# Kernel tuning notes

Measured on AMD Instinct MI355X. Metric: run time of the kernel, lower is better.

## Reference

```python
import jax, jax.numpy as jnp
from jax import lax
import numpy as np

B, T, F, H, L, HOR = 512, 512, 16, 256, 3, 24


def setup_inputs() -> dict:
    key = jax.random.key(0)
    ks = jax.random.split(key, 9)
    s = 0.05
    x = jax.random.normal(ks[0], (B, T, F), dtype=jnp.float32)
    # PyTorch LSTM params: gate order (i, f, g, o), W_ih [4H, in], W_hh [4H, H]
    W_ih0 = jax.random.normal(ks[1], (4 * H, F), dtype=jnp.float32) * s
    W_ih12 = jax.random.normal(ks[2], (L - 1, 4 * H, H), dtype=jnp.float32) * s
    W_hh = jax.random.normal(ks[3], (L, 4 * H, H), dtype=jnp.float32) * s
    b_ih = jax.random.normal(ks[4], (L, 4 * H), dtype=jnp.float32) * s
    b_hh = jax.random.normal(ks[5], (L, 4 * H), dtype=jnp.float32) * s
    fc_W = jax.random.normal(ks[6], (HOR, H), dtype=jnp.float32) * s
    fc_b = jax.random.normal(ks[7], (HOR,), dtype=jnp.float32) * s
    return {"x": x, "W_ih0": W_ih0, "W_ih12": W_ih12, "W_hh": W_hh,
            "b_ih": b_ih, "b_hh": b_hh, "fc_W": fc_W, "fc_b": fc_b}


def _lstm_layer(x, W_ih, W_hh, b_ih, b_hh):
    # x: [B, T, in] -> h sequence [B, T, H]
    Bn = x.shape[0]
    Hn = W_hh.shape[1]
    # precompute input contribution for all timesteps (one big GEMM)
    xg = jnp.einsum('bti,gi->btg', x, W_ih) + b_ih  # [B, T, 4H]
    W_hh_T = W_hh.T  # [H, 4H]

    def step(carry, xg_t):
        h, c = carry
        gates = xg_t + h @ W_hh_T + b_hh  # [B, 4H]
        i, f, g, o = jnp.split(gates, 4, axis=-1)
        c = jax.nn.sigmoid(f) * c + jax.nn.sigmoid(i) * jnp.tanh(g)
        h = jax.nn.sigmoid(o) * jnp.tanh(c)
        return (h, c), h

    h0 = jnp.zeros((Bn, Hn), x.dtype)
    c0 = jnp.zeros((Bn, Hn), x.dtype)
    _, hs = lax.scan(step, (h0, c0), jnp.swapaxes(xg, 0, 1))  # [T, B, H]
    return jnp.swapaxes(hs, 0, 1)


def reference(x, W_ih0, W_ih12, W_hh, b_ih, b_hh, fc_W, fc_b):
    h = _lstm_layer(x, W_ih0, W_hh[0], b_ih[0], b_hh[0])
    for l in range(1, L):
        h = _lstm_layer(h, W_ih12[l - 1], W_hh[l], b_ih[l], b_hh[l])
    last_hidden = h[:, -1, :]  # [B, H]
    return last_hidden @ fc_W.T + fc_b  # [B, horizon]
```

## Files before the change

### kernel.cpp

```cpp
#include <hip/hip_runtime.h>
#include <hip/hip_bf16.h>
#include <stdint.h>

#define Bsz 512
#define Tsz 512
#define Fsz 16
#define Hsz 256
#define HORZ 24

#define NG 8
#define NBT 8
#define BT 64
#define USL 32
#define PD 8
#define HBUF_ELEMS ((size_t)3*PD*Bsz*Hsz)
#define NFLAGS (3*NG*NBT)
#define AROW_B 512
#define ABUF_B (BT*AROW_B)
#define HTILE_B (BT*64)
#define SMEM_B (3*ABUF_B + HTILE_B)

#define POISON   0x7FC07FC0u
#define POISON64 0x7FC07FC07FC07FC0ull

typedef float  f32x4  __attribute__((ext_vector_type(4)));
typedef float  f32x16 __attribute__((ext_vector_type(16)));
typedef __bf16 bf16x8 __attribute__((ext_vector_type(8)));
typedef uint32_t u32x2 __attribute__((ext_vector_type(2)));
typedef uint32_t u32x4 __attribute__((ext_vector_type(4)));

__device__ __forceinline__ float sigm(float v){ return 1.f/(1.f+__expf(-v)); }

__device__ __forceinline__ bf16x8 ld_sc01_b128(const void* p){
  bf16x8 r;
  asm volatile("global_load_dwordx4 %0, %1, off sc0 sc1" : "=&v"(r) : "v"(p) : "memory");
  return r;
}
__device__ __forceinline__ u32x2 ld_b64_async(const void* p){
  u32x2 r;
  asm volatile("global_load_dwordx2 %0, %1, off" : "=&v"(r) : "v"(p) : "memory");
  return r;
}
__device__ __forceinline__ void st_sc01_b64(void* p, uint64_t v){
  asm volatile("global_store_dwordx2 %0, %1, off sc0 sc1" :: "v"(p), "v"(v) : "memory");
}
__device__ __forceinline__ void st_sc01_b32(void* p, uint32_t v){
  asm volatile("global_store_dword %0, %1, off sc0 sc1" :: "v"(p), "v"(v) : "memory");
}
__device__ __forceinline__ uint32_t ld_sc01_b32(const void* p){
  uint32_t r;
  asm volatile("global_load_dword %0, %1, off sc0 sc1\n\ts_waitcnt vmcnt(0)"
    : "=&v"(r) : "v"(p) : "memory");
  return r;
}
__device__ __forceinline__ void wait_flag(const unsigned int* fp, int target){
  int guard = 0;
  while ((int)ld_sc01_b32(fp) < target){
    __builtin_amdgcn_s_sleep(1);
    if (++guard > (1<<18)) break;
  }
}
__device__ __forceinline__ bool poison_free(const bf16x8* v){
  bool ok = true;
  #pragma unroll
  for (int j=0;j<4;++j){
    u32x4 uv = __builtin_bit_cast(u32x4, v[j]);
    ok = ok && (uv[0] != POISON) && (uv[2] != POISON);
  }
  return ok;
}
__device__ __forceinline__ void poll_load4(bf16x8* dst, const __bf16* src){
  int guard = 0;
  for(;;){
    #pragma unroll
    for (int j=0;j<4;++j) dst[j] = ld_sc01_b128(src + j*8);
    asm volatile("s_waitcnt vmcnt(0)" ::: "memory");
    __builtin_amdgcn_sched_barrier(0);
    if (poison_free(dst)) break;
    __builtin_amdgcn_s_sleep(1);
    if (++guard > (1<<16)) break;
  }
}

template<bool L0>
__device__ __forceinline__ void lstm_body(
    int l, int g, int nb, int tid,
    const float* __restrict__ xin,
    const float* __restrict__ Wih0,
    const float* __restrict__ Wih12,
    const float* __restrict__ Whh,
    const float* __restrict__ bih,
    const float* __restrict__ bhh,
    __bf16* __restrict__ hb,
    unsigned int* __restrict__ flags,
    char* smem)
{
  char* ain0  = smem;
  char* ain1  = smem + ABUF_B;
  char* hrc   = smem + 2*ABUF_B;
  char* htile = smem + 3*ABUF_B;

  const int lane = tid & 63;
  const int wid  = tid >> 6;
  const int wm   = wid >> 2;
  const int wn   = wid & 3;
  const int b0   = nb * BT;
  const int m0   = wm * 32;
  const int n0   = wn * 32;

  const int colL = n0 + (lane & 31);
  const int hi   = lane >> 5;
  const int kg8  = hi * 8;
  const int kg16 = hi * 16;
  const int R    = (colL&3)*Hsz + g*USL + (colL>>2);
  const float bias = bih[l*4*Hsz + R] + bhh[l*4*Hsz + R];
  const int rowA = m0 + (lane & 31);
  const int swzA = (rowA & 7) << 4;

  constexpr int NC = L0 ? 17 : 32;
  bf16x8 w[NC];
  {
    const float* recB = Whh + ((size_t)l*4*Hsz + R)*Hsz;
    #pragma unroll
    for (int c=0;c<NC;++c){
      const float* p;
      if constexpr (L0) p = (c==0) ? (Wih0 + (size_t)R*Fsz + kg8)
                                   : (recB + (c-1)*16 + kg8);
      else              p = (c<16) ? (Wih12 + ((size_t)(l-1)*4*Hsz + R)*Hsz + c*16 + kg8)
                                   : (recB + (c-16)*16 + kg8);
      f32x4 u0 = *(const f32x4*)p;
      f32x4 u1 = *(const f32x4*)(p+4);
      bf16x8 t;
      #pragma unroll
      for (int j=0;j<4;++j){ t[j]=(__bf16)u0[j]; t[j+4]=(__bf16)u1[j]; }
      w[c] = t;
    }
  }

  const int srow = tid >> 3, sq = tid & 7;
  const int sswz = (srow & 7) << 4;
  const size_t sgrow = (size_t)(b0 + srow) * Hsz;

  float cst[16];
  #pragma unroll
  for (int i=0;i<16;++i) cst[i]=0.f;

  unsigned int* myflag = flags + ((l*NG+g)*NBT + nb);
  const bool q2 = ((colL & 3) == 2);
  auto slotp = [&](int ll, int s){ return hb + ((size_t)ll*PD + (s&(PD-1)))*Bsz*Hsz; };

  {
    u32x4 z = {0,0,0,0};
    #pragma unroll
    for (int j=0;j<4;++j) *(u32x4*)(hrc + tid*64 + j*16) = z;
  }
  if constexpr (L0){
    u32x2 xv = ld_b64_async(xin + ((size_t)(b0+srow)*Tsz + 0)*Fsz + sq*2);
    asm volatile("s_waitcnt vmcnt(0)" ::: "memory");
    __builtin_amdgcn_sched_barrier(0);
    char* d = ain0 + srow*32 + sq*4;
    *(__bf16*)(d)   = (__bf16)__uint_as_float(xv[0]);
    *(__bf16*)(d+2) = (__bf16)__uint_as_float(xv[1]);
  } else {
    bf16x8 av[4];
    poll_load4(av, slotp(l-1,0) + sgrow + sq*32);
    #pragma unroll
    for (int j=0;j<4;++j)
      *(bf16x8*)(ain0 + srow*AROW_B + ((sq*64 + j*16) ^ sswz)) = av[j];
  }
  __syncthreads();

  for (int t=0; t<Tsz; ++t){
    char* aprd = (t&1) ? ain1 : ain0;
    char* apwr = (t&1) ? ain0 : ain1;

    if (l < 2 && (t & 3) == 0 && t >= 4 && tid < 8)
      wait_flag(flags + (((l+1)*NG + tid)*NBT + nb), t-3);

    bf16x8 hiv[4]; const __bf16* pfsrc = nullptr;
    const bool pfon = (!L0) && (t+1 < Tsz);
    if constexpr (L0){
      u32x2 xv = ld_b64_async(xin + ((size_t)(b0+srow)*Tsz + t)*Fsz + sq*2);
      bf16x8 hrv[4];
      if (t > 0) poll_load4(hrv, slotp(l,t-1) + sgrow + sq*32);
      else { asm volatile("s_waitcnt vmcnt(0)" ::: "memory");
             __builtin_amdgcn_sched_barrier(0); }
      char* d = ain0 + srow*32 + sq*4;
      *(__bf16*)(d)   = (__bf16)__uint_as_float(xv[0]);
      *(__bf16*)(d+2) = (__bf16)__uint_as_float(xv[1]);
      if (t > 0){
        #pragma unroll
        for (int j=0;j<4;++j)
          *(bf16x8*)(hrc + srow*AROW_B + ((sq*64 + j*16) ^ sswz)) = hrv[j];
      }
    } else {
      if (t > 0){
        bf16x8 hrv[4];
        poll_load4(hrv, slotp(l,t-1) + sgrow + sq*32);
        #pragma unroll
        for (int j=0;j<4;++j)
          *(bf16x8*)(hrc + srow*AROW_B + ((sq*64 + j*16) ^ sswz)) = hrv[j];
      }
      if (pfon){
        pfsrc = slotp(l-1,t+1) + sgrow + sq*32;
        #pragma unroll
        for (int j=0;j<4;++j) hiv[j] = ld_sc01_b128(pfsrc + j*8);
      }
    }
    __syncthreads();

    f32x16 acc;
    #pragma unroll
    for (int i=0;i<16;++i) acc[i]=0.f;
    #pragma unroll
    for (int c=0;c<NC;++c){
      bf16x8 af;
      if constexpr (L0){
        if (c==0) af = *(const bf16x8*)(ain0 + rowA*32 + kg16);
        else      af = *(const bf16x8*)(hrc + rowA*AROW_B + ((((c-1)*32) + kg16) ^ swzA));
      } else {
        if (c<16) af = *(const bf16x8*)(aprd + rowA*AROW_B + (((c*32) + kg16) ^ swzA));
        else      af = *(const bf16x8*)(hrc  + rowA*AROW_B + ((((c-16)*32) + kg16) ^ swzA));
      }
      acc = __builtin_amdgcn_mfma_f32_32x32x16_bf16(af, w[c], acc, 0,0,0);
    }

    #pragma unroll
    for (int i=0;i<16;++i){
      float v  = acc[i] + bias;
      float vv = q2 ? 2.f*v : v;
      float sg = sigm(vv);
      float act = q2 ? (2.f*sg - 1.f) : sg;
      float a1 = __shfl_xor(act,1,64);
      float a2 = __shfl_xor(act,2,64);
      float a3 = __shfl_xor(act,3,64);
      if ((lane&3)==0){
        float cn = a1*cst[i] + act*a2;
        cst[i] = cn;
        float th = 2.f*sigm(2.f*cn) - 1.f;
        float hv = a3*th;
        int r = (i&3) + 8*(i>>2) + 4*hi;
        int unit = colL >> 2;
        *(__bf16*)(htile + (m0 + r)*64 + unit*2) = (__bf16)hv;
      }
    }
    __syncthreads();

    if (pfon){
      asm volatile("s_waitcnt vmcnt(0)" ::: "memory");
      __builtin_amdgcn_sched_barrier(0);
      if (!poison_free(hiv)) poll_load4(hiv, pfsrc);
      #pragma unroll
      for (int j=0;j<4;++j)
        *(bf16x8*)(apwr + srow*AROW_B + ((sq*64 + j*16) ^ sswz)) = hiv[j];
    }
    __syncthreads();
    {
      uint64_t v = *(const uint64_t*)(htile + srow*64 + sq*8);
      st_sc01_b64(slotp(l,t)   + sgrow + g*USL + sq*4, v);
      st_sc01_b64(slotp(l,t+2) + sgrow + g*USL + sq*4, POISON64);
    }
    if (tid==0) st_sc01_b32(myflag, (uint32_t)(t+1));
  }
}

__global__ __launch_bounds__(512, 2) void lstm_persist(
    const float* __restrict__ xin,
    const float* __restrict__ Wih0,
    const float* __restrict__ Wih12,
    const float* __restrict__ Whh,
    const float* __restrict__ bih,
    const float* __restrict__ bhh,
    __bf16* __restrict__ hb,
    unsigned int* __restrict__ flags)
{
  __shared__ __align__(16) char smem[SMEM_B];
  const int bid = blockIdx.x;
  const int l   = bid >> 6;
  const int g   = (bid >> 3) & 7;
  const int nb  = bid & 7;
  const int tid = threadIdx.x;
  if (l == 0)
    lstm_body<true >(l,g,nb,tid, xin,Wih0,Wih12,Whh,bih,bhh, hb,flags, smem);
  else
    lstm_body<false>(l,g,nb,tid, xin,Wih0,Wih12,Whh,bih,bhh, hb,flags, smem);
}

__global__ void init_ws(uint32_t* __restrict__ hb32, uint32_t* __restrict__ flags)
{
  size_t i = (size_t)blockIdx.x*blockDim.x + threadIdx.x;
  size_t n = (HBUF_ELEMS*2)/16;
  if (i < n){
    u32x4 v = {POISON, POISON, POISON, POISON};
    *(u32x4*)(hb32 + i*4) = v;
  }
  if (i < NFLAGS) flags[i] = 0;
}

__global__ void fc_kernel(const __bf16* __restrict__ hb,
                          const float* __restrict__ fcW,
                          const float* __restrict__ fcb,
                          float* __restrict__ out)
{
  __shared__ float hs[Hsz];
  int b = blockIdx.x;
  const __bf16* hp = hb + ((size_t)(2*PD + ((Tsz-1)&(PD-1))))*Bsz*Hsz + (size_t)b*Hsz;
  for (int i = threadIdx.x; i < Hsz; i += 64) hs[i] = (float)hp[i];
  __syncthreads();
  int o = threadIdx.x;
  if (o < HORZ) {
    float a = fcb[o];
    #pragma unroll 8
    for (int u=0; u<Hsz; ++u) a += hs[u]*fcW[o*Hsz + u];
    out[b*HORZ + o] = a;
  }
}

extern "C" void kernel_launch(void* const* d_in, const int* in_sizes, int n_in,
                              void* d_out, int out_size, void* d_ws, size_t ws_size,
                              hipStream_t stream)
{
  const float* x     = (const float*)d_in[0];
  const float* Wih0  = (const float*)d_in[1];
  const float* Wih12 = (const float*)d_in[2];
  const float* Whh   = (const float*)d_in[3];
  const float* bih   = (const float*)d_in[4];
  const float* bhh   = (const float*)d_in[5];
  const float* fcW   = (const float*)d_in[6];
  const float* fcb   = (const float*)d_in[7];

  __bf16* hb = (__bf16*)d_ws;
  unsigned int* flags = (unsigned int*)((char*)d_ws + HBUF_ELEMS*2);

  size_t nchunk = (HBUF_ELEMS*2)/16;
  int ib = (int)((nchunk + 255) / 256);
  hipLaunchKernelGGL(init_ws, dim3(ib), dim3(256), 0, stream, (uint32_t*)hb, flags);

  hipLaunchKernelGGL(lstm_persist, dim3(3*NG*NBT), dim3(512), 0, stream,
                     x, Wih0, Wih12, Whh, bih, bhh, hb, flags);
  hipLaunchKernelGGL(fc_kernel, dim3(Bsz), dim3(64), 0, stream, hb, fcW, fcb, (float*)d_out);
}
```

Baseline: 3.283 ms.

## Split batch tile into two half-tiles with interleaved prefetch and 16x16 MFMAs

Each timestep now processes the 64-row batch tile as two 32-row halves, using 16x16x32 MFMAs in place of 32x32x16. While one half computes, the global loads for the other half's recurrent state and input are issued early, so polling latency overlaps with compute. The poison slot written ahead moves from t+2 to t+1, and the shared-memory layout is rebuilt with per-half buffers. The risks are more barriers per step, a changed poison and prefetch protocol that may race, and different register pressure.

```diff
diff --git a/kernel.cpp b/kernel.cpp
--- a/kernel.cpp
+++ b/kernel.cpp
@@ -11,22 +11,18 @@
 #define NG 8
 #define NBT 8
 #define BT 64
+#define HR 32
 #define USL 32
 #define PD 8
 #define HBUF_ELEMS ((size_t)3*PD*Bsz*Hsz)
 #define NFLAGS (3*NG*NBT)
-#define AROW_B 512
-#define ABUF_B (BT*AROW_B)
-#define HTILE_B (BT*64)
-#define SMEM_B (3*ABUF_B + HTILE_B)
+#define SMEM_B (84*1024)
 
 #define POISON   0x7FC07FC0u
 #define POISON64 0x7FC07FC07FC07FC0ull
 
 typedef float  f32x4  __attribute__((ext_vector_type(4)));
-typedef float  f32x16 __attribute__((ext_vector_type(16)));
 typedef __bf16 bf16x8 __attribute__((ext_vector_type(8)));
-typedef uint32_t u32x2 __attribute__((ext_vector_type(2)));
 typedef uint32_t u32x4 __attribute__((ext_vector_type(4)));
 
 __device__ __forceinline__ float sigm(float v){ return 1.f/(1.f+__expf(-v)); }
@@ -36,9 +32,9 @@
   asm volatile("global_load_dwordx4 %0, %1, off sc0 sc1" : "=&v"(r) : "v"(p) : "memory");
   return r;
 }
-__device__ __forceinline__ u32x2 ld_b64_async(const void* p){
-  u32x2 r;
-  asm volatile("global_load_dwordx2 %0, %1, off" : "=&v"(r) : "v"(p) : "memory");
+__device__ __forceinline__ uint32_t ld_b32_async(const void* p){
+  uint32_t r;
+  asm volatile("global_load_dword %0, %1, off" : "=&v"(r) : "v"(p) : "memory");
   return r;
 }
 __device__ __forceinline__ void st_sc01_b64(void* p, uint64_t v){
@@ -60,27 +56,105 @@
     if (++guard > (1<<18)) break;
   }
 }
-__device__ __forceinline__ bool poison_free(const bf16x8* v){
-  bool ok = true;
-  #pragma unroll
-  for (int j=0;j<4;++j){
-    u32x4 uv = __builtin_bit_cast(u32x4, v[j]);
-    ok = ok && (uv[0] != POISON) && (uv[2] != POISON);
-  }
-  return ok;
-}
-__device__ __forceinline__ void poll_load4(bf16x8* dst, const __bf16* src){
+__device__ __forceinline__ bool pf_ok2(const bf16x8* v){
+  u32x4 a = __builtin_bit_cast(u32x4, v[0]);
+  u32x4 b = __builtin_bit_cast(u32x4, v[1]);
+  return (a[0]!=POISON) & (a[2]!=POISON) & (b[0]!=POISON) & (b[2]!=POISON);
+}
+__device__ __forceinline__ void poll_load2(bf16x8* d, const __bf16* src){
   int guard = 0;
   for(;;){
-    #pragma unroll
-    for (int j=0;j<4;++j) dst[j] = ld_sc01_b128(src + j*8);
+    d[0] = ld_sc01_b128(src);
+    d[1] = ld_sc01_b128(src + 8);
     asm volatile("s_waitcnt vmcnt(0)" ::: "memory");
     __builtin_amdgcn_sched_barrier(0);
-    if (poison_free(dst)) break;
+    if (pf_ok2(d)) break;
     __builtin_amdgcn_s_sleep(1);
     if (++guard > (1<<16)) break;
   }
 }
+
+#define HALF_ITER(T, TY, RB, RBN, HRCX, AINX, HTX, CSTX, HRV, HIV, XV, HRVN, HIVN, XVN) \
+  {                                                                                     \
+    if ((T) > 0){                                                                       \
+      asm volatile("s_waitcnt vmcnt(0)" ::: "memory");                                  \
+      __builtin_amdgcn_sched_barrier(0);                                                \
+      if (!pf_ok2(HRV))                                                                 \
+        poll_load2(HRV, slotp(l,(T)-1) + (size_t)(b0+(RB)+sr)*Hsz + sq*16);             \
+      *(bf16x8*)((HRCX) + sr*512 + ((sq*32)    ^ skey)) = (HRV)[0];                     \
+      *(bf16x8*)((HRCX) + sr*512 + ((sq*32+16) ^ skey)) = (HRV)[1];                     \
+      if constexpr (L0){                                                                \
+        *(__bf16*)((AINX) + sr*64 + sq*2) = (__bf16)__uint_as_float(XV);                \
+      } else {                                                                          \
+        if (!pf_ok2(HIV))                                                               \
+          poll_load2(HIV, slotp(l-1,(T)) + (size_t)(b0+(RB)+sr)*Hsz + sq*16);           \
+        *(bf16x8*)((AINX) + sr*512 + ((sq*32)    ^ skey)) = (HIV)[0];                   \
+        *(bf16x8*)((AINX) + sr*512 + ((sq*32+16) ^ skey)) = (HIV)[1];                   \
+      }                                                                                 \
+    }                                                                                   \
+    __syncthreads();                                                                    \
+    f32x4 acc0, acc1;                                                                   \
+    acc0[0]=0.f;acc0[1]=0.f;acc0[2]=0.f;acc0[3]=0.f;                                    \
+    acc1[0]=0.f;acc1[1]=0.f;acc1[2]=0.f;acc1[3]=0.f;                                    \
+    _Pragma("unroll")                                                                   \
+    for (int c=0;c<NC;++c){                                                             \
+      bf16x8 a0, a1;                                                                    \
+      if constexpr (L0){                                                                \
+        if (c==0){ a0 = *(const bf16x8*)((AINX) + r0*64 + kq16);                        \
+                   a1 = *(const bf16x8*)((AINX) + r1*64 + kq16); }                      \
+        else { int off = (((c-1)*64) + kq16) ^ akey;                                    \
+               a0 = *(const bf16x8*)((HRCX) + r0*512 + off);                            \
+               a1 = *(const bf16x8*)((HRCX) + r1*512 + off); }                          \
+      } else {                                                                          \
+        const char* bse = (c<8) ? (AINX) : (HRCX);                                     \
+        int cc = (c<8) ? c : c-8;                                                       \
+        int off = ((cc*64) + kq16) ^ akey;                                              \
+        a0 = *(const bf16x8*)(bse + r0*512 + off);                                      \
+        a1 = *(const bf16x8*)(bse + r1*512 + off);                                      \
+      }                                                                                 \
+      acc0 = __builtin_amdgcn_mfma_f32_16x16x32_bf16(a0, w[c], acc0, 0,0,0);            \
+      acc1 = __builtin_amdgcn_mfma_f32_16x16x32_bf16(a1, w[c], acc1, 0,0,0);            \
+    }                                                                                   \
+    _Pragma("unroll")                                                                   \
+    for (int mt=0; mt<2; ++mt){                                                         \
+      _Pragma("unroll")                                                                 \
+      for (int rr=0; rr<4; ++rr){                                                       \
+        float v  = (mt ? acc1[rr] : acc0[rr]) + bias;                                   \
+        float vv = q2 ? 2.f*v : v;                                                      \
+        float sg = sigm(vv);                                                            \
+        float act = q2 ? (2.f*sg - 1.f) : sg;                                           \
+        float a1f = __shfl_xor(act,1,64);                                               \
+        float a2f = __shfl_xor(act,2,64);                                               \
+        float a3f = __shfl_xor(act,3,64);                                               \
+        if (gate==0){                                                                   \
+          float cn = a1f*(CSTX)[mt*4+rr] + act*a2f;                                     \
+          (CSTX)[mt*4+rr] = cn;                                                         \
+          float hv = a3f*(2.f*sigm(2.f*cn) - 1.f);                                      \
+          int rh = mt*16 + kq*4 + rr;                                                   \
+          *(__bf16*)((HTX) + rh*64 + unit*2) = (__bf16)hv;                              \
+        }                                                                               \
+      }                                                                                 \
+    }                                                                                   \
+    __syncthreads();                                                                    \
+    if (tid < 256){                                                                     \
+      int row = tid>>3, q = tid&7;                                                      \
+      uint64_t v = *(const uint64_t*)((HTX) + row*64 + q*8);                            \
+      st_sc01_b64(slotp(l,(T))   + (size_t)(b0+(RB)+row)*Hsz + g*USL + q*4, v);         \
+      st_sc01_b64(slotp(l,(T)+1) + (size_t)(b0+(RB)+row)*Hsz + g*USL + q*4, POISON64);  \
+    }                                                                                   \
+    if ((TY) >= 1 && (TY) < Tsz){                                                       \
+      const __bf16* pa = slotp(l,(TY)-1) + (size_t)(b0+(RBN)+sr)*Hsz + sq*16;           \
+      (HRVN)[0] = ld_sc01_b128(pa);                                                     \
+      (HRVN)[1] = ld_sc01_b128(pa + 8);                                                 \
+      if constexpr (L0){                                                                \
+        XVN = ld_b32_async(xin + ((size_t)(b0+(RBN)+sr)*Tsz + (TY))*Fsz + sq);          \
+      } else {                                                                          \
+        const __bf16* pb = slotp(l-1,(TY)) + (size_t)(b0+(RBN)+sr)*Hsz + sq*16;         \
+        (HIVN)[0] = ld_sc01_b128(pb);                                                   \
+        (HIVN)[1] = ld_sc01_b128(pb + 8);                                               \
+      }                                                                                 \
+    }                                                                                   \
+  }
 
 template<bool L0>
 __device__ __forceinline__ void lstm_body(
@@ -95,171 +169,104 @@
     unsigned int* __restrict__ flags,
     char* smem)
 {
-  char* ain0  = smem;
-  char* ain1  = smem + ABUF_B;
-  char* hrc   = smem + 2*ABUF_B;
-  char* htile = smem + 3*ABUF_B;
+  constexpr int ASZ = L0 ? (HR*64) : (HR*512);
+  char* hrc0 = smem;
+  char* hrc1 = smem + HR*512;
+  char* ain0 = smem + 2*HR*512;
+  char* ain1 = ain0 + ASZ;
+  char* ht0  = ain1 + ASZ;
+  char* ht1  = ht0 + HR*64;
 
   const int lane = tid & 63;
   const int wid  = tid >> 6;
-  const int wm   = wid >> 2;
-  const int wn   = wid & 3;
   const int b0   = nb * BT;
-  const int m0   = wm * 32;
-  const int n0   = wn * 32;
-
-  const int colL = n0 + (lane & 31);
-  const int hi   = lane >> 5;
-  const int kg8  = hi * 8;
-  const int kg16 = hi * 16;
-  const int R    = (colL&3)*Hsz + g*USL + (colL>>2);
+  const int colL = wid*16 + (lane & 15);
+  const int kq   = lane >> 4;
+  const int kq16 = kq * 16;
+  const int gate = colL & 3;
+  const int unit = colL >> 2;
+  const int R    = gate*Hsz + g*USL + unit;
   const float bias = bih[l*4*Hsz + R] + bhh[l*4*Hsz + R];
-  const int rowA = m0 + (lane & 31);
-  const int swzA = (rowA & 7) << 4;
-
-  constexpr int NC = L0 ? 17 : 32;
+  const bool q2 = (gate == 2);
+  const int r0 = lane & 15, r1 = 16 + (lane & 15);
+  const int akey = (lane & 7) << 4;
+
+  const int sr = tid >> 4, sq = tid & 15;
+  const int skey = (sr & 7) << 4;
+
+  constexpr int NC = L0 ? 9 : 16;
+  const int kg8 = kq * 8;
   bf16x8 w[NC];
   {
     const float* recB = Whh + ((size_t)l*4*Hsz + R)*Hsz;
     #pragma unroll
     for (int c=0;c<NC;++c){
-      const float* p;
-      if constexpr (L0) p = (c==0) ? (Wih0 + (size_t)R*Fsz + kg8)
-                                   : (recB + (c-1)*16 + kg8);
-      else              p = (c<16) ? (Wih12 + ((size_t)(l-1)*4*Hsz + R)*Hsz + c*16 + kg8)
-                                   : (recB + (c-16)*16 + kg8);
-      f32x4 u0 = *(const f32x4*)p;
-      f32x4 u1 = *(const f32x4*)(p+4);
       bf16x8 t;
-      #pragma unroll
-      for (int j=0;j<4;++j){ t[j]=(__bf16)u0[j]; t[j+4]=(__bf16)u1[j]; }
+      if constexpr (L0){
+        if (c==0){
+          if (kg8 < Fsz){
+            const float* p = Wih0 + (size_t)R*Fsz + kg8;
+            #pragma unroll
+            for (int j=0;j<8;++j) t[j] = (__bf16)p[j];
+          } else {
+            #pragma unroll
+            for (int j=0;j<8;++j) t[j] = (__bf16)0.f;
+          }
+        } else {
+          const float* p = recB + (c-1)*32 + kg8;
+          #pragma unroll
+          for (int j=0;j<8;++j) t[j] = (__bf16)p[j];
+        }
+      } else {
+        const float* p = (c<8) ? (Wih12 + ((size_t)(l-1)*4*Hsz + R)*Hsz + c*32 + kg8)
+                               : (recB + (c-8)*32 + kg8);
+        #pragma unroll
+        for (int j=0;j<8;++j) t[j] = (__bf16)p[j];
+      }
       w[c] = t;
     }
   }
 
-  const int srow = tid >> 3, sq = tid & 7;
-  const int sswz = (srow & 7) << 4;
-  const size_t sgrow = (size_t)(b0 + srow) * Hsz;
-
-  float cst[16];
+  float cst0[8], cst1[8];
   #pragma unroll
-  for (int i=0;i<16;++i) cst[i]=0.f;
+  for (int i=0;i<8;++i){ cst0[i]=0.f; cst1[i]=0.f; }
 
   unsigned int* myflag = flags + ((l*NG+g)*NBT + nb);
-  const bool q2 = ((colL & 3) == 2);
   auto slotp = [&](int ll, int s){ return hb + ((size_t)ll*PD + (s&(PD-1)))*Bsz*Hsz; };
 
   {
     u32x4 z = {0,0,0,0};
     #pragma unroll
-    for (int j=0;j<4;++j) *(u32x4*)(hrc + tid*64 + j*16) = z;
+    for (int j=0;j<4;++j) *(u32x4*)(smem + tid*64 + j*16) = z;
   }
   if constexpr (L0){
-    u32x2 xv = ld_b64_async(xin + ((size_t)(b0+srow)*Tsz + 0)*Fsz + sq*2);
-    asm volatile("s_waitcnt vmcnt(0)" ::: "memory");
-    __builtin_amdgcn_sched_barrier(0);
-    char* d = ain0 + srow*32 + sq*4;
-    *(__bf16*)(d)   = (__bf16)__uint_as_float(xv[0]);
-    *(__bf16*)(d+2) = (__bf16)__uint_as_float(xv[1]);
+    *(uint64_t*)(ain0 + tid*8) = 0;
+    __syncthreads();
+    float xa = xin[((size_t)(b0 +      sr)*Tsz + 0)*Fsz + sq];
+    float xb = xin[((size_t)(b0 + HR + sr)*Tsz + 0)*Fsz + sq];
+    *(__bf16*)(ain0 + sr*64 + sq*2) = (__bf16)xa;
+    *(__bf16*)(ain1 + sr*64 + sq*2) = (__bf16)xb;
   } else {
-    bf16x8 av[4];
-    poll_load4(av, slotp(l-1,0) + sgrow + sq*32);
-    #pragma unroll
-    for (int j=0;j<4;++j)
-      *(bf16x8*)(ain0 + srow*AROW_B + ((sq*64 + j*16) ^ sswz)) = av[j];
+    bf16x8 tmp[2];
+    poll_load2(tmp, slotp(l-1,0) + (size_t)(b0 + sr)*Hsz + sq*16);
+    *(bf16x8*)(ain0 + sr*512 + ((sq*32)    ^ skey)) = tmp[0];
+    *(bf16x8*)(ain0 + sr*512 + ((sq*32+16) ^ skey)) = tmp[1];
+    poll_load2(tmp, slotp(l-1,0) + (size_t)(b0 + HR + sr)*Hsz + sq*16);
+    *(bf16x8*)(ain1 + sr*512 + ((sq*32)    ^ skey)) = tmp[0];
+    *(bf16x8*)(ain1 + sr*512 + ((sq*32+16) ^ skey)) = tmp[1];
   }
   __syncthreads();
 
+  bf16x8 hrvA[2], hrvB[2], hivA[2], hivB[2];
+  uint32_t xvA=0, xvB=0;
+
   for (int t=0; t<Tsz; ++t){
-    char* aprd = (t&1) ? ain1 : ain0;
-    char* apwr = (t&1) ? ain0 : ain1;
-
     if (l < 2 && (t & 3) == 0 && t >= 4 && tid < 8)
       wait_flag(flags + (((l+1)*NG + tid)*NBT + nb), t-3);
 
-    bf16x8 hiv[4]; const __bf16* pfsrc = nullptr;
-    const bool pfon = (!L0) && (t+1 < Tsz);
-    if constexpr (L0){
-      u32x2 xv = ld_b64_async(xin + ((size_t)(b0+srow)*Tsz + t)*Fsz + sq*2);
-      bf16x8 hrv[4];
-      if (t > 0) poll_load4(hrv, slotp(l,t-1) + sgrow + sq*32);
-      else { asm volatile("s_waitcnt vmcnt(0)" ::: "memory");
-             __builtin_amdgcn_sched_barrier(0); }
-      char* d = ain0 + srow*32 + sq*4;
-      *(__bf16*)(d)   = (__bf16)__uint_as_float(xv[0]);
-      *(__bf16*)(d+2) = (__bf16)__uint_as_float(xv[1]);
-      if (t > 0){
-        #pragma unroll
-        for (int j=0;j<4;++j)
-          *(bf16x8*)(hrc + srow*AROW_B + ((sq*64 + j*16) ^ sswz)) = hrv[j];
-      }
-    } else {
-      if (t > 0){
-        bf16x8 hrv[4];
-        poll_load4(hrv, slotp(l,t-1) + sgrow + sq*32);
-        #pragma unroll
-        for (int j=0;j<4;++j)
-          *(bf16x8*)(hrc + srow*AROW_B + ((sq*64 + j*16) ^ sswz)) = hrv[j];
-      }
-      if (pfon){
-        pfsrc = slotp(l-1,t+1) + sgrow + sq*32;
-        #pragma unroll
-        for (int j=0;j<4;++j) hiv[j] = ld_sc01_b128(pfsrc + j*8);
-      }
-    }
-    __syncthreads();
-
-    f32x16 acc;
-    #pragma unroll
-    for (int i=0;i<16;++i) acc[i]=0.f;
-    #pragma unroll
-    for (int c=0;c<NC;++c){
-      bf16x8 af;
-      if constexpr (L0){
-        if (c==0) af = *(const bf16x8*)(ain0 + rowA*32 + kg16);
-        else      af = *(const bf16x8*)(hrc + rowA*AROW_B + ((((c-1)*32) + kg16) ^ swzA));
-      } else {
-        if (c<16) af = *(const bf16x8*)(aprd + rowA*AROW_B + (((c*32) + kg16) ^ swzA));
-        else      af = *(const bf16x8*)(hrc  + rowA*AROW_B + ((((c-16)*32) + kg16) ^ swzA));
-      }
-      acc = __builtin_amdgcn_mfma_f32_32x32x16_bf16(af, w[c], acc, 0,0,0);
-    }
-
-    #pragma unroll
-    for (int i=0;i<16;++i){
-      float v  = acc[i] + bias;
-      float vv = q2 ? 2.f*v : v;
-      float sg = sigm(vv);
-      float act = q2 ? (2.f*sg - 1.f) : sg;
-      float a1 = __shfl_xor(act,1,64);
-      float a2 = __shfl_xor(act,2,64);
-      float a3 = __shfl_xor(act,3,64);
-      if ((lane&3)==0){
-        float cn = a1*cst[i] + act*a2;
-        cst[i] = cn;
-        float th = 2.f*sigm(2.f*cn) - 1.f;
-        float hv = a3*th;
-        int r = (i&3) + 8*(i>>2) + 4*hi;
-        int unit = colL >> 2;
-        *(__bf16*)(htile + (m0 + r)*64 + unit*2) = (__bf16)hv;
-      }
-    }
-    __syncthreads();
-
-    if (pfon){
-      asm volatile("s_waitcnt vmcnt(0)" ::: "memory");
-      __builtin_amdgcn_sched_barrier(0);
-      if (!poison_free(hiv)) poll_load4(hiv, pfsrc);
-      #pragma unroll
-      for (int j=0;j<4;++j)
-        *(bf16x8*)(apwr + srow*AROW_B + ((sq*64 + j*16) ^ sswz)) = hiv[j];
-    }
-    __syncthreads();
-    {
-      uint64_t v = *(const uint64_t*)(htile + srow*64 + sq*8);
-      st_sc01_b64(slotp(l,t)   + sgrow + g*USL + sq*4, v);
-      st_sc01_b64(slotp(l,t+2) + sgrow + g*USL + sq*4, POISON64);
-    }
+    HALF_ITER(t, t,   0,  HR, hrc0, ain0, ht0, cst0, hrvA, hivA, xvA, hrvB, hivB, xvB);
+    HALF_ITER(t, t+1, HR, 0,  hrc1, ain1, ht1, cst1, hrvB, hivB, xvB, hrvA, hivA, xvA);
+
     if (tid==0) st_sc01_b32(myflag, (uint32_t)(t+1));
   }
 }
```

Result: slower. 3.508 ms (+6.9%).

## Process two batch tiles per block and overlap one tile's loads with other's compute

Applied to the files above, without the earlier changes.

Each persistent block now owns two 64-row batch tiles (X and Y) instead of one, halving the grid to 96 blocks. Within each timestep the block alternates tiles, issuing the global loads for the other tile's recurrent and input state before computing the current tile, so the exchange latency is hidden behind MFMA work. This also amortizes the register-resident weights over twice the batch. The cost is more shared memory per block (136KB), fewer blocks in flight, and a longer serial chain per timestep in each block.

```diff
diff --git a/kernel.cpp b/kernel.cpp
--- a/kernel.cpp
+++ b/kernel.cpp
@@ -9,16 +9,13 @@
 #define HORZ 24
 
 #define NG 8
-#define NBT 8
+#define NPAIR 4
 #define BT 64
 #define USL 32
 #define PD 8
 #define HBUF_ELEMS ((size_t)3*PD*Bsz*Hsz)
-#define NFLAGS (3*NG*NBT)
-#define AROW_B 512
-#define ABUF_B (BT*AROW_B)
-#define HTILE_B (BT*64)
-#define SMEM_B (3*ABUF_B + HTILE_B)
+#define NFLAGS (3*NG*NPAIR)
+#define SMEM_B (136*1024)
 
 #define POISON   0x7FC07FC0u
 #define POISON64 0x7FC07FC07FC07FC0ull
@@ -82,9 +79,89 @@
   }
 }
 
+#define TILE_INT(T, CHK, ISS, TO, B0C, B0O, HRC_, AIN_, HT_, CST_, PFR, PFI, XV, PFRO, PFIO, XVO) \
+{                                                                                       \
+  if (CHK){                                                                             \
+    asm volatile("s_waitcnt vmcnt(0)" ::: "memory");                                    \
+    __builtin_amdgcn_sched_barrier(0);                                                  \
+    if (!poison_free(PFR))                                                              \
+      poll_load4(PFR, slotp(l,(T)-1) + (size_t)((B0C)+srow)*Hsz + sq*32);               \
+    _Pragma("unroll")                                                                   \
+    for (int j=0;j<4;++j)                                                               \
+      *(bf16x8*)((HRC_) + srow*512 + ((sq*64 + j*16) ^ sswz)) = (PFR)[j];               \
+    if constexpr (L0){                                                                  \
+      char* d_ = (AIN_) + srow*32 + sq*4;                                               \
+      *(__bf16*)(d_)   = (__bf16)__uint_as_float((XV)[0]);                              \
+      *(__bf16*)(d_+2) = (__bf16)__uint_as_float((XV)[1]);                              \
+    } else {                                                                            \
+      if (!poison_free(PFI))                                                            \
+        poll_load4(PFI, slotp(l-1,(T)) + (size_t)((B0C)+srow)*Hsz + sq*32);             \
+      _Pragma("unroll")                                                                 \
+      for (int j=0;j<4;++j)                                                             \
+        *(bf16x8*)((AIN_) + srow*512 + ((sq*64 + j*16) ^ sswz)) = (PFI)[j];             \
+    }                                                                                   \
+  }                                                                                     \
+  if (ISS){                                                                             \
+    const __bf16* pr_ = slotp(l,(TO)-1) + (size_t)((B0O)+srow)*Hsz + sq*32;             \
+    _Pragma("unroll")                                                                   \
+    for (int j=0;j<4;++j) (PFRO)[j] = ld_sc01_b128(pr_ + j*8);                          \
+    if constexpr (L0){                                                                  \
+      XVO = ld_b64_async(xin + ((size_t)((B0O)+srow)*Tsz + (TO))*Fsz + sq*2);           \
+    } else {                                                                            \
+      const __bf16* pi_ = slotp(l-1,(TO)) + (size_t)((B0O)+srow)*Hsz + sq*32;           \
+      _Pragma("unroll")                                                                 \
+      for (int j=0;j<4;++j) (PFIO)[j] = ld_sc01_b128(pi_ + j*8);                        \
+    }                                                                                   \
+  }                                                                                     \
+  __syncthreads();                                                                      \
+  {                                                                                     \
+    f32x16 acc;                                                                         \
+    _Pragma("unroll")                                                                   \
+    for (int i=0;i<16;++i) acc[i]=0.f;                                                  \
+    _Pragma("unroll")                                                                   \
+    for (int c=0;c<NC;++c){                                                             \
+      bf16x8 af;                                                                        \
+      if constexpr (L0){                                                                \
+        if (c==0) af = *(const bf16x8*)((AIN_) + rowA*32 + kg16);                       \
+        else      af = *(const bf16x8*)((HRC_) + rowA*512 + ((((c-1)*32) + kg16) ^ swzA)); \
+      } else {                                                                          \
+        if (c<16) af = *(const bf16x8*)((AIN_) + rowA*512 + (((c*32) + kg16) ^ swzA));  \
+        else      af = *(const bf16x8*)((HRC_) + rowA*512 + ((((c-16)*32) + kg16) ^ swzA)); \
+      }                                                                                 \
+      acc = __builtin_amdgcn_mfma_f32_32x32x16_bf16(af, w[c], acc, 0,0,0);              \
+    }                                                                                   \
+    _Pragma("unroll")                                                                   \
+    for (int i=0;i<16;++i){                                                             \
+      float v  = acc[i] + bias;                                                         \
+      float vv = q2 ? 2.f*v : v;                                                        \
+      float sg = sigm(vv);                                                              \
+      float act = q2 ? (2.f*sg - 1.f) : sg;                                             \
+      float a1f = __shfl_xor(act,1,64);                                                 \
+      float a2f = __shfl_xor(act,2,64);                                                 \
+      float a3f = __shfl_xor(act,3,64);                                                 \
+      if ((lane&3)==0){                                                                 \
+        float cn = a1f*(CST_)[i] + act*a2f;                                             \
+        (CST_)[i] = cn;                                                                 \
+        float th = 2.f*sigm(2.f*cn) - 1.f;                                              \
+        float hv = a3f*th;                                                              \
+        int r_ = (i&3) + 8*(i>>2) + 4*hi;                                               \
+        int unit_ = colL >> 2;                                                          \
+        *(__bf16*)((HT_) + (m0 + r_)*64 + unit_*2) = (__bf16)hv;                        \
+      }                                                                                 \
+    }                                                                                   \
+  }                                                                                     \
+  __syncthreads();                                                                      \
+  {                                                                                     \
+    int row_ = tid>>3, q_ = tid&7;                                                      \
+    uint64_t v_ = *(const uint64_t*)((HT_) + row_*64 + q_*8);                           \
+    st_sc01_b64(slotp(l,(T))   + (size_t)((B0C)+row_)*Hsz + g*USL + q_*4, v_);          \
+    st_sc01_b64(slotp(l,(T)+2) + (size_t)((B0C)+row_)*Hsz + g*USL + q_*4, POISON64);    \
+  }                                                                                     \
+}
+
 template<bool L0>
 __device__ __forceinline__ void lstm_body(
-    int l, int g, int nb, int tid,
+    int l, int g, int p, int tid,
     const float* __restrict__ xin,
     const float* __restrict__ Wih0,
     const float* __restrict__ Wih12,
@@ -95,16 +172,19 @@
     unsigned int* __restrict__ flags,
     char* smem)
 {
-  char* ain0  = smem;
-  char* ain1  = smem + ABUF_B;
-  char* hrc   = smem + 2*ABUF_B;
-  char* htile = smem + 3*ABUF_B;
+  char* hrcX = smem;
+  char* hrcY = smem + 32*1024;
+  char* ainX = smem + 64*1024;
+  char* ainY = smem + 96*1024;
+  char* htX  = smem + 128*1024;
+  char* htY  = smem + 132*1024;
 
   const int lane = tid & 63;
   const int wid  = tid >> 6;
   const int wm   = wid >> 2;
   const int wn   = wid & 3;
-  const int b0   = nb * BT;
+  const int b0x  = p * 128;
+  const int b0y  = p * 128 + 64;
   const int m0   = wm * 32;
   const int n0   = wn * 32;
 
@@ -116,6 +196,7 @@
   const float bias = bih[l*4*Hsz + R] + bhh[l*4*Hsz + R];
   const int rowA = m0 + (lane & 31);
   const int swzA = (rowA & 7) << 4;
+  const bool q2 = ((colL & 3) == 2);
 
   constexpr int NC = L0 ? 17 : 32;
   bf16x8 w[NC];
@@ -123,13 +204,13 @@
     const float* recB = Whh + ((size_t)l*4*Hsz + R)*Hsz;
     #pragma unroll
     for (int c=0;c<NC;++c){
-      const float* p;
-      if constexpr (L0) p = (c==0) ? (Wih0 + (size_t)R*Fsz + kg8)
-                                   : (recB + (c-1)*16 + kg8);
-      else              p = (c<16) ? (Wih12 + ((size_t)(l-1)*4*Hsz + R)*Hsz + c*16 + kg8)
-                                   : (recB + (c-16)*16 + kg8);
-      f32x4 u0 = *(const f32x4*)p;
-      f32x4 u1 = *(const f32x4*)(p+4);
+      const float* pw;
+      if constexpr (L0) pw = (c==0) ? (Wih0 + (size_t)R*Fsz + kg8)
+                                    : (recB + (c-1)*16 + kg8);
+      else              pw = (c<16) ? (Wih12 + ((size_t)(l-1)*4*Hsz + R)*Hsz + c*16 + kg8)
+                                    : (recB + (c-16)*16 + kg8);
+      f32x4 u0 = *(const f32x4*)pw;
+      f32x4 u1 = *(const f32x4*)(pw+4);
       bf16x8 t;
       #pragma unroll
       for (int j=0;j<4;++j){ t[j]=(__bf16)u0[j]; t[j+4]=(__bf16)u1[j]; }
@@ -139,127 +220,55 @@
 
   const int srow = tid >> 3, sq = tid & 7;
   const int sswz = (srow & 7) << 4;
-  const size_t sgrow = (size_t)(b0 + srow) * Hsz;
-
-  float cst[16];
+
+  float cstX[16], cstY[16];
   #pragma unroll
-  for (int i=0;i<16;++i) cst[i]=0.f;
-
-  unsigned int* myflag = flags + ((l*NG+g)*NBT + nb);
-  const bool q2 = ((colL & 3) == 2);
+  for (int i=0;i<16;++i){ cstX[i]=0.f; cstY[i]=0.f; }
+
+  unsigned int* myflag = flags + ((l*NG+g)*NPAIR + p);
   auto slotp = [&](int ll, int s){ return hb + ((size_t)ll*PD + (s&(PD-1)))*Bsz*Hsz; };
 
   {
     u32x4 z = {0,0,0,0};
     #pragma unroll
-    for (int j=0;j<4;++j) *(u32x4*)(hrc + tid*64 + j*16) = z;
+    for (int j=0;j<8;++j) *(u32x4*)(smem + tid*128 + j*16) = z;
   }
   if constexpr (L0){
-    u32x2 xv = ld_b64_async(xin + ((size_t)(b0+srow)*Tsz + 0)*Fsz + sq*2);
+    u32x2 xa = ld_b64_async(xin + ((size_t)(b0x+srow)*Tsz + 0)*Fsz + sq*2);
+    u32x2 xb = ld_b64_async(xin + ((size_t)(b0y+srow)*Tsz + 0)*Fsz + sq*2);
     asm volatile("s_waitcnt vmcnt(0)" ::: "memory");
     __builtin_amdgcn_sched_barrier(0);
-    char* d = ain0 + srow*32 + sq*4;
-    *(__bf16*)(d)   = (__bf16)__uint_as_float(xv[0]);
-    *(__bf16*)(d+2) = (__bf16)__uint_as_float(xv[1]);
+    char* da = ainX + srow*32 + sq*4;
+    char* db = ainY + srow*32 + sq*4;
+    *(__bf16*)(da)   = (__bf16)__uint_as_float(xa[0]);
+    *(__bf16*)(da+2) = (__bf16)__uint_as_float(xa[1]);
+    *(__bf16*)(db)   = (__bf16)__uint_as_float(xb[0]);
+    *(__bf16*)(db+2) = (__bf16)__uint_as_float(xb[1]);
   } else {
-    bf16x8 av[4];
-    poll_load4(av, slotp(l-1,0) + sgrow + sq*32);
+    bf16x8 tp[4];
+    poll_load4(tp, slotp(l-1,0) + (size_t)(b0x+srow)*Hsz + sq*32);
     #pragma unroll
     for (int j=0;j<4;++j)
-      *(bf16x8*)(ain0 + srow*AROW_B + ((sq*64 + j*16) ^ sswz)) = av[j];
+      *(bf16x8*)(ainX + srow*512 + ((sq*64 + j*16) ^ sswz)) = tp[j];
+    poll_load4(tp, slotp(l-1,0) + (size_t)(b0y+srow)*Hsz + sq*32);
+    #pragma unroll
+    for (int j=0;j<4;++j)
+      *(bf16x8*)(ainY + srow*512 + ((sq*64 + j*16) ^ sswz)) = tp[j];
   }
   __syncthreads();
 
+  bf16x8 pfrX[4], pfiX[4], pfrY[4], pfiY[4];
+  u32x2 xvX, xvY;
+
   for (int t=0; t<Tsz; ++t){
-    char* aprd = (t&1) ? ain1 : ain0;
-    char* apwr = (t&1) ? ain0 : ain1;
-
     if (l < 2 && (t & 3) == 0 && t >= 4 && tid < 8)
-      wait_flag(flags + (((l+1)*NG + tid)*NBT + nb), t-3);
-
-    bf16x8 hiv[4]; const __bf16* pfsrc = nullptr;
-    const bool pfon = (!L0) && (t+1 < Tsz);
-    if constexpr (L0){
-      u32x2 xv = ld_b64_async(xin + ((size_t)(b0+srow)*Tsz + t)*Fsz + sq*2);
-      bf16x8 hrv[4];
-      if (t > 0) poll_load4(hrv, slotp(l,t-1) + sgrow + sq*32);
-      else { asm volatile("s_waitcnt vmcnt(0)" ::: "memory");
-             __builtin_amdgcn_sched_barrier(0); }
-      char* d = ain0 + srow*32 + sq*4;
-      *(__bf16*)(d)   = (__bf16)__uint_as_float(xv[0]);
-      *(__bf16*)(d+2) = (__bf16)__uint_as_float(xv[1]);
-      if (t > 0){
-        #pragma unroll
-        for (int j=0;j<4;++j)
-          *(bf16x8*)(hrc + srow*AROW_B + ((sq*64 + j*16) ^ sswz)) = hrv[j];
-      }
-    } else {
-      if (t > 0){
-        bf16x8 hrv[4];
-        poll_load4(hrv, slotp(l,t-1) + sgrow + sq*32);
-        #pragma unroll
-        for (int j=0;j<4;++j)
-          *(bf16x8*)(hrc + srow*AROW_B + ((sq*64 + j*16) ^ sswz)) = hrv[j];
-      }
-      if (pfon){
-        pfsrc = slotp(l-1,t+1) + sgrow + sq*32;
-        #pragma unroll
-        for (int j=0;j<4;++j) hiv[j] = ld_sc01_b128(pfsrc + j*8);
-      }
-    }
-    __syncthreads();
-
-    f32x16 acc;
-    #pragma unroll
-    for (int i=0;i<16;++i) acc[i]=0.f;
-    #pragma unroll
-    for (int c=0;c<NC;++c){
-      bf16x8 af;
-      if constexpr (L0){
-        if (c==0) af = *(const bf16x8*)(ain0 + rowA*32 + kg16);
-        else      af = *(const bf16x8*)(hrc + rowA*AROW_B + ((((c-1)*32) + kg16) ^ swzA));
-      } else {
-        if (c<16) af = *(const bf16x8*)(aprd + rowA*AROW_B + (((c*32) + kg16) ^ swzA));
-        else      af = *(const bf16x8*)(hrc  + rowA*AROW_B + ((((c-16)*32) + kg16) ^ swzA));
-      }
-      acc = __builtin_amdgcn_mfma_f32_32x32x16_bf16(af, w[c], acc, 0,0,0);
-    }
-
-    #pragma unroll
-    for (int i=0;i<16;++i){
-      float v  = acc[i] + bias;
-      float vv = q2 ? 2.f*v : v;
-      float sg = sigm(vv);
-      float act = q2 ? (2.f*sg - 1.f) : sg;
-      float a1 = __shfl_xor(act,1,64);
-      float a2 = __shfl_xor(act,2,64);
-      float a3 = __shfl_xor(act,3,64);
-      if ((lane&3)==0){
-        float cn = a1*cst[i] + act*a2;
-        cst[i] = cn;
-        float th = 2.f*sigm(2.f*cn) - 1.f;
-        float hv = a3*th;
-        int r = (i&3) + 8*(i>>2) + 4*hi;
-        int unit = colL >> 2;
-        *(__bf16*)(htile + (m0 + r)*64 + unit*2) = (__bf16)hv;
-      }
-    }
-    __syncthreads();
-
-    if (pfon){
-      asm volatile("s_waitcnt vmcnt(0)" ::: "memory");
-      __builtin_amdgcn_sched_barrier(0);
-      if (!poison_free(hiv)) poll_load4(hiv, pfsrc);
-      #pragma unroll
-      for (int j=0;j<4;++j)
-        *(bf16x8*)(apwr + srow*AROW_B + ((sq*64 + j*16) ^ sswz)) = hiv[j];
-    }
-    __syncthreads();
-    {
-      uint64_t v = *(const uint64_t*)(htile + srow*64 + sq*8);
-      st_sc01_b64(slotp(l,t)   + sgrow + g*USL + sq*4, v);
-      st_sc01_b64(slotp(l,t+2) + sgrow + g*USL + sq*4, POISON64);
-    }
+      wait_flag(flags + (((l+1)*NG + tid)*NPAIR + p), t-3);
+
+    TILE_INT(t, (t>0), (t>0), t,
+             b0x, b0y, hrcX, ainX, htX, cstX, pfrX, pfiX, xvX, pfrY, pfiY, xvY);
+    TILE_INT(t, (t>0), (t+1<Tsz), t+1,
+             b0y, b0x, hrcY, ainY, htY, cstY, pfrY, pfiY, xvY, pfrX, pfiX, xvX);
+
     if (tid==0) st_sc01_b32(myflag, (uint32_t)(t+1));
   }
 }
@@ -276,14 +285,14 @@
 {
   __shared__ __align__(16) char smem[SMEM_B];
   const int bid = blockIdx.x;
-  const int l   = bid >> 6;
-  const int g   = (bid >> 3) & 7;
-  const int nb  = bid & 7;
+  const int l   = bid >> 5;
+  const int g   = (bid >> 2) & 7;
+  const int p   = bid & 3;
   const int tid = threadIdx.x;
   if (l == 0)
-    lstm_body<true >(l,g,nb,tid, xin,Wih0,Wih12,Whh,bih,bhh, hb,flags, smem);
+    lstm_body<true >(l,g,p,tid, xin,Wih0,Wih12,Whh,bih,bhh, hb,flags, smem);
   else
-    lstm_body<false>(l,g,nb,tid, xin,Wih0,Wih12,Whh,bih,bhh, hb,flags, smem);
+    lstm_body<false>(l,g,p,tid, xin,Wih0,Wih12,Whh,bih,bhh, hb,flags, smem);
 }
 
 __global__ void init_ws(uint32_t* __restrict__ hb32, uint32_t* __restrict__ flags)
@@ -336,7 +345,7 @@
   int ib = (int)((nchunk + 255) / 256);
   hipLaunchKernelGGL(init_ws, dim3(ib), dim3(256), 0, stream, (uint32_t*)hb, flags);
 
-  hipLaunchKernelGGL(lstm_persist, dim3(3*NG*NBT), dim3(512), 0, stream,
+  hipLaunchKernelGGL(lstm_persist, dim3(3*NG*NPAIR), dim3(512), 0, stream,
                      x, Wih0, Wih12, Whh, bih, bhh, hb, flags);
   hipLaunchKernelGGL(fc_kernel, dim3(Bsz), dim3(64), 0, stream, hb, fcW, fcb, (float*)d_out);
 }
```

New measurement: 10.12 ms. 208% more time.

## Drop double-buffered input prefetch; issue recurrent and input loads together

Applied to the files above, without the earlier changes.

Removes the double-buffered lower-layer input prefetch (ain0/ain1) and instead loads the current step's lower-layer h and the recurrent h in one batch, with a single vmcnt wait and a poison check before falling back to polling. This eliminates one __syncthreads per timestep and the separate prefetch phase, and shrinks LDS to one input buffer (the shared-memory size is padded to a fixed 84KB). The trade-off is that the input load is no longer hidden behind the previous step's compute, so it may stall on the producer layer's critical path. The larger fixed LDS footprint may also affect occupancy at two blocks per CU.

```diff
diff --git a/kernel.cpp b/kernel.cpp
--- a/kernel.cpp
+++ b/kernel.cpp
@@ -18,7 +18,7 @@
 #define AROW_B 512
 #define ABUF_B (BT*AROW_B)
 #define HTILE_B (BT*64)
-#define SMEM_B (3*ABUF_B + HTILE_B)
+#define SMEM_B (84*1024)
 
 #define POISON   0x7FC07FC0u
 #define POISON64 0x7FC07FC07FC07FC0ull
@@ -95,10 +95,9 @@
     unsigned int* __restrict__ flags,
     char* smem)
 {
-  char* ain0  = smem;
-  char* ain1  = smem + ABUF_B;
-  char* hrc   = smem + 2*ABUF_B;
-  char* htile = smem + 3*ABUF_B;
+  char* ain   = smem;
+  char* hrc   = smem + ABUF_B;
+  char* htile = smem + 2*ABUF_B;
 
   const int lane = tid & 63;
   const int wid  = tid >> 6;
@@ -154,38 +153,24 @@
     #pragma unroll
     for (int j=0;j<4;++j) *(u32x4*)(hrc + tid*64 + j*16) = z;
   }
-  if constexpr (L0){
-    u32x2 xv = ld_b64_async(xin + ((size_t)(b0+srow)*Tsz + 0)*Fsz + sq*2);
-    asm volatile("s_waitcnt vmcnt(0)" ::: "memory");
-    __builtin_amdgcn_sched_barrier(0);
-    char* d = ain0 + srow*32 + sq*4;
-    *(__bf16*)(d)   = (__bf16)__uint_as_float(xv[0]);
-    *(__bf16*)(d+2) = (__bf16)__uint_as_float(xv[1]);
-  } else {
-    bf16x8 av[4];
-    poll_load4(av, slotp(l-1,0) + sgrow + sq*32);
-    #pragma unroll
-    for (int j=0;j<4;++j)
-      *(bf16x8*)(ain0 + srow*AROW_B + ((sq*64 + j*16) ^ sswz)) = av[j];
-  }
   __syncthreads();
 
   for (int t=0; t<Tsz; ++t){
-    char* aprd = (t&1) ? ain1 : ain0;
-    char* apwr = (t&1) ? ain0 : ain1;
-
     if (l < 2 && (t & 3) == 0 && t >= 4 && tid < 8)
       wait_flag(flags + (((l+1)*NG + tid)*NBT + nb), t-3);
 
-    bf16x8 hiv[4]; const __bf16* pfsrc = nullptr;
-    const bool pfon = (!L0) && (t+1 < Tsz);
+    bf16x8 hrv[4];
+    const __bf16* hrsrc = slotp(l,t-1) + sgrow + sq*32;
     if constexpr (L0){
       u32x2 xv = ld_b64_async(xin + ((size_t)(b0+srow)*Tsz + t)*Fsz + sq*2);
-      bf16x8 hrv[4];
-      if (t > 0) poll_load4(hrv, slotp(l,t-1) + sgrow + sq*32);
-      else { asm volatile("s_waitcnt vmcnt(0)" ::: "memory");
-             __builtin_amdgcn_sched_barrier(0); }
-      char* d = ain0 + srow*32 + sq*4;
+      if (t > 0){
+        #pragma unroll
+        for (int j=0;j<4;++j) hrv[j] = ld_sc01_b128(hrsrc + j*8);
+      }
+      asm volatile("s_waitcnt vmcnt(0)" ::: "memory");
+      __builtin_amdgcn_sched_barrier(0);
+      if (t > 0 && !poison_free(hrv)) poll_load4(hrv, hrsrc);
+      char* d = ain + srow*32 + sq*4;
       *(__bf16*)(d)   = (__bf16)__uint_as_float(xv[0]);
       *(__bf16*)(d+2) = (__bf16)__uint_as_float(xv[1]);
       if (t > 0){
@@ -194,18 +179,26 @@
           *(bf16x8*)(hrc + srow*AROW_B + ((sq*64 + j*16) ^ sswz)) = hrv[j];
       }
     } else {
+      bf16x8 hivv[4];
+      const __bf16* hisrc = slotp(l-1,t) + sgrow + sq*32;
       if (t > 0){
-        bf16x8 hrv[4];
-        poll_load4(hrv, slotp(l,t-1) + sgrow + sq*32);
+        #pragma unroll
+        for (int j=0;j<4;++j) hrv[j] = ld_sc01_b128(hrsrc + j*8);
+      }
+      #pragma unroll
+      for (int j=0;j<4;++j) hivv[j] = ld_sc01_b128(hisrc + j*8);
+      asm volatile("s_waitcnt vmcnt(0)" ::: "memory");
+      __builtin_amdgcn_sched_barrier(0);
+      if (t > 0 && !poison_free(hrv)) poll_load4(hrv, hrsrc);
+      if (!poison_free(hivv))         poll_load4(hivv, hisrc);
+      if (t > 0){
         #pragma unroll
         for (int j=0;j<4;++j)
           *(bf16x8*)(hrc + srow*AROW_B + ((sq*64 + j*16) ^ sswz)) = hrv[j];
       }
-      if (pfon){
-        pfsrc = slotp(l-1,t+1) + sgrow + sq*32;
-        #pragma unroll
-        for (int j=0;j<4;++j) hiv[j] = ld_sc01_b128(pfsrc + j*8);
-      }
+      #pragma unroll
+      for (int j=0;j<4;++j)
+        *(bf16x8*)(ain + srow*AROW_B + ((sq*64 + j*16) ^ sswz)) = hivv[j];
     }
     __syncthreads();
 
@@ -216,11 +209,11 @@
     for (int c=0;c<NC;++c){
       bf16x8 af;
       if constexpr (L0){
-        if (c==0) af = *(const bf16x8*)(ain0 + rowA*32 + kg16);
+        if (c==0) af = *(const bf16x8*)(ain + rowA*32 + kg16);
         else      af = *(const bf16x8*)(hrc + rowA*AROW_B + ((((c-1)*32) + kg16) ^ swzA));
       } else {
-        if (c<16) af = *(const bf16x8*)(aprd + rowA*AROW_B + (((c*32) + kg16) ^ swzA));
-        else      af = *(const bf16x8*)(hrc  + rowA*AROW_B + ((((c-16)*32) + kg16) ^ swzA));
+        if (c<16) af = *(const bf16x8*)(ain + rowA*AROW_B + (((c*32) + kg16) ^ swzA));
+        else      af = *(const bf16x8*)(hrc + rowA*AROW_B + ((((c-16)*32) + kg16) ^ swzA));
       }
       acc = __builtin_amdgcn_mfma_f32_32x32x16_bf16(af, w[c], acc, 0,0,0);
     }
@@ -246,15 +239,6 @@
     }
     __syncthreads();
 
-    if (pfon){
-      asm volatile("s_waitcnt vmcnt(0)" ::: "memory");
-      __builtin_amdgcn_sched_barrier(0);
-      if (!poison_free(hiv)) poll_load4(hiv, pfsrc);
-      #pragma unroll
-      for (int j=0;j<4;++j)
-        *(bf16x8*)(apwr + srow*AROW_B + ((sq*64 + j*16) ^ sswz)) = hiv[j];
-    }
-    __syncthreads();
     {
       uint64_t v = *(const uint64_t*)(htile + srow*64 + sq*8);
       st_sc01_b64(slotp(l,t)   + sgrow + g*USL + sq*4, v);
@@ -262,6 +246,7 @@
     }
     if (tid==0) st_sc01_b32(myflag, (uint32_t)(t+1));
   }
+  asm volatile("s_waitcnt vmcnt(0)" ::: "memory");
 }
 
 __global__ __launch_bounds__(512, 2) void lstm_persist(
```

Result: slower. 3.767 ms (+14.7%).
